# Kernel tuning notes

Measured on AMD Instinct MI355X. Metric: run time of the kernel, lower is better.

The kernel has to match this reference:

```python
import jax, jax.numpy as jnp
import numpy as np

HID = 128
NLAYERS = 8
LAT = 32
DIM_IN = 63 + 15 + LAT  # pe(xyz,L=10)=3+60, pe(shift,L=2)=3+12, latent=32 -> 110


def _pe(x, L):
    # NeRF positional encoding, include_input=True, freq-major [sin3,cos3] per freq
    freqs = (2.0 ** jnp.arange(L)).astype(x.dtype)
    xf = x[..., None, :] * freqs[:, None]                      # [..., L, 3]
    sc = jnp.concatenate([jnp.sin(xf), jnp.cos(xf)], axis=-1)  # [..., L, 6]
    return jnp.concatenate([x, sc.reshape(*x.shape[:-1], 6 * L)], axis=-1)


def setup_inputs() -> dict:
    key = jax.random.key(0)
    ks = jax.random.split(key, 24)
    B, P, V = 2, 32768, 5023
    d = {}
    d["pts"] = jax.random.normal(ks[0], (B, P, 3), jnp.float32)
    d["deformed_mesh_pts"] = jax.random.normal(ks[1], (B, V, 3), jnp.float32)
    d["cano_verts"] = jax.random.normal(ks[2], (1, V, 3), jnp.float32)
    d["motion_latent"] = jax.random.normal(ks[3], (B, P, LAT), jnp.float32)
    for i in range(NLAYERS):
        fin = DIM_IN if i == 0 else (DIM_IN + HID if i == NLAYERS // 2 else HID)
        d[f"w{i}"] = jax.random.normal(ks[4 + i], (HID, fin), jnp.float32) / np.sqrt(fin).astype(np.float32)
        d[f"b{i}"] = jnp.zeros((HID,), jnp.float32)
    d["w_out"] = jax.random.normal(ks[20], (3, HID), jnp.float32) * 0.01
    d["b_out"] = jnp.zeros((3,), jnp.float32)
    return d


def reference(pts, deformed_mesh_pts, cano_verts, motion_latent,
              w0, b0, w1, b1, w2, b2, w3, b3, w4, b4, w5, b5, w6, b6, w7, b7,
              w_out, b_out):
    # mesh-guided shift per vertex
    mesh_shift = cano_verts - deformed_mesh_pts                 # [B,V,3]
    # point-to-point NN search (squared euclidean cdist + argmin)
    d2 = ((pts ** 2).sum(-1)[:, :, None]
          + (deformed_mesh_pts ** 2).sum(-1)[:, None, :]
          - 2.0 * jnp.einsum('bpc,bvc->bpv', pts, deformed_mesh_pts))  # [B,P,V]
    d2 = jnp.maximum(d2, 0.0)
    idx = jnp.argmin(d2, axis=-1)                               # [B,P]
    dist = jnp.min(d2, axis=-1)                                 # [B,P]
    weight = jnp.exp(-dist)[..., None]                          # 1/exp(dist)
    gidx = jnp.broadcast_to(idx[:, :, None], idx.shape + (3,))
    gshift = jnp.take_along_axis(mesh_shift, gidx, axis=1) * weight  # [B,P,3]
    # deformation MLP with skip connection at layer 4
    initial = jnp.concatenate([_pe(pts, 10), _pe(gshift, 2), motion_latent], axis=-1)
    ws = [w0, w1, w2, w3, w4, w5, w6, w7]
    bs = [b0, b1, b2, b3, b4, b5, b6, b7]
    x = initial
    last_feat = x
    for i in range(NLAYERS):
        inp = jnp.concatenate([initial, x], axis=-1) if i == NLAYERS // 2 else x
        x = inp @ ws[i].T + bs[i]
        last_feat = x  # pre-activation feature (out_feat_ls[-1])
        x = jax.nn.relu(x)
    mlp_shift = x @ w_out.T + b_out                             # [B,P,3]
    pts_shifts = gshift + mlp_shift
    return pts + pts_shifts, last_feat
```

## Files before the change

### kernel.cpp

```cpp
#include <hip/hip_runtime.h>
#include <math.h>

typedef unsigned short ushort_t;
typedef unsigned int   uint_t;
typedef __attribute__((ext_vector_type(8)))  short bf16x8;
typedef __attribute__((ext_vector_type(16))) float f32x16;

#define NPTS   65536
#define NV     5023
#define NVP    5120
#define NTILE  160
#define LATD   32
#define KF     110
#define FSTR   112
#define MARGIN 1.5e-2f

union U4 { uint_t u[4]; bf16x8 v; };

__device__ __forceinline__ ushort_t f2bf(float f) {
  union { float f; unsigned u; } x; x.f = f;
  unsigned r = x.u + 0x7fffu + ((x.u >> 16) & 1u);
  return (ushort_t)(r >> 16);
}
__device__ __forceinline__ float bf2f(ushort_t u) {
  union { unsigned u; float f; } x; x.u = ((unsigned)u) << 16;
  return x.f;
}
__device__ __forceinline__ uint_t packsplit(float v) {
  const ushort_t h = f2bf(v);
  const ushort_t l = f2bf(v - bf2f(h));
  return (uint_t)h | ((uint_t)l << 16);
}

__device__ __forceinline__ void dbl_step(float& s, float& c) {
  const float t = s * c;
  const float cn = fmaf(-2.f * s, s, 1.f);
  s = t + t;
  c = cn;
}

__global__ __launch_bounds__(256) void k_prep(
    const float* __restrict__ dm,
    const float* __restrict__ w0, const float* __restrict__ w1,
    const float* __restrict__ w2, const float* __restrict__ w3,
    const float* __restrict__ w4, const float* __restrict__ w5,
    const float* __restrict__ w6, const float* __restrict__ w7,
    ushort_t* __restrict__ wsWh, ushort_t* __restrict__ wsWl,
    ushort_t* __restrict__ aFF, ushort_t* __restrict__ aFH,
    float4* __restrict__ vq)
{
  const int e = blockIdx.x * 256 + threadIdx.x;
  {
    const int p = e >> 14, local = e & 16383;
    const int j   = local & 7;
    const int lh  = (local >> 3) & 1;
    const int l31 = (local >> 4) & 31;
    const int tn  = (local >> 9) & 3;
    const int ks  = (local >> 11) & 7;
    const int n = tn*32 + l31;
    const int k = ks*16 + lh*8 + j;
    float v;
    if (p == 0)      v = (k < KF) ? w0[n*110 + k] : 0.f;
    else if (p == 1) v = w1[n*128 + k];
    else if (p == 2) v = w2[n*128 + k];
    else if (p == 3) v = w3[n*128 + k];
    else if (p == 4) v = (k < KF) ? w4[n*238 + k] : 0.f;
    else if (p == 5) v = w4[n*238 + KF + k];
    else if (p == 6) v = w5[n*128 + k];
    else if (p == 7) v = w6[n*128 + k];
    else             v = w7[n*128 + k];
    const ushort_t h = f2bf(v);
    wsWh[e] = h;
    wsWl[e] = f2bf(v - bf2f(h));
  }
  if (e < 2*NVP) {
    const int b = (e >= NVP) ? 1 : 0;
    const int v = e - b*NVP;
    const float* __restrict__ dmb = dm + b*NV*3;
    float x = 0.f, y = 0.f, z = 0.f, wv = 3.0e38f;
    if (v < NV) {
      x = dmb[v*3+0]; y = dmb[v*3+1]; z = dmb[v*3+2];
      wv = fmaf(x,x, fmaf(y,y, z*z));
    }
    const ushort_t hx = f2bf(x),  hy = f2bf(y),  hz = f2bf(z),  hw = f2bf(wv);
    const ushort_t lx = f2bf(x - bf2f(hx)), ly = f2bf(y - bf2f(hy));
    const ushort_t lz = f2bf(z - bf2f(hz)), lw = f2bf(wv - bf2f(hw));
    U4 F, H;
    F.u[0] = (uint_t)hx | ((uint_t)hy << 16);
    F.u[1] = (uint_t)hz | ((uint_t)hw << 16);
    F.u[2] = (uint_t)lx | ((uint_t)ly << 16);
    F.u[3] = (uint_t)lz | ((uint_t)lw << 16);
    H.u[0] = F.u[0]; H.u[1] = F.u[1]; H.u[2] = 0; H.u[3] = 0;
    *(bf16x8*)(aFF + (size_t)e*8) = F.v;
    *(bf16x8*)(aFH + (size_t)e*8) = H.v;
    vq[e] = make_float4(x, y, z, wv);
  }
}

__device__ __forceinline__ float min16(const f32x16& d) {
  const float t0 = fminf(fminf(d[0],d[1]),   fminf(d[2],d[3]));
  const float t1 = fminf(fminf(d[4],d[5]),   fminf(d[6],d[7]));
  const float t2 = fminf(fminf(d[8],d[9]),   fminf(d[10],d[11]));
  const float t3 = fminf(fminf(d[12],d[13]), fminf(d[14],d[15]));
  return fminf(fminf(t0,t1), fminf(t2,t3));
}

__global__ __launch_bounds__(256, 2) void k_nnfeat(
    const float* __restrict__ pts, const float* __restrict__ dm,
    const float* __restrict__ cano, const float* __restrict__ lat,
    const ushort_t* __restrict__ aFF, const ushort_t* __restrict__ aFH,
    const float4* __restrict__ vq,
    uint_t* __restrict__ feat, float* __restrict__ base3)
{
  __shared__ float sD[128];
  __shared__ int   sI[128];

  const int tid = threadIdx.x;
  const int lane = tid & 63, w = tid >> 6;
  const int l31 = lane & 31, lh = lane >> 5;
  const int g0 = blockIdx.x * 128;
  const int b  = blockIdx.x >> 8;
  const int pt = g0 + w*32 + l31;

  const float px = pts[pt*3+0], py = pts[pt*3+1], pz = pts[pt*3+2];
  const float p2 = fmaf(px,px, fmaf(py,py, pz*pz));

  const float tpx = -2.f*px, tpy = -2.f*py, tpz = -2.f*pz;
  const ushort_t hpx = f2bf(tpx), hpy = f2bf(tpy), hpz = f2bf(tpz);
  const ushort_t lpx = f2bf(tpx - bf2f(hpx));
  const ushort_t lpy = f2bf(tpy - bf2f(hpy));
  const ushort_t lpz = f2bf(tpz - bf2f(hpz));
  U4 Bh, Bl;
  Bh.u[0] = (uint_t)hpx | ((uint_t)hpy << 16);
  Bh.u[1] = (uint_t)hpz | (0x3F80u << 16);
  Bh.u[2] = Bh.u[0]; Bh.u[3] = Bh.u[1];
  Bl.u[0] = (uint_t)lpx | ((uint_t)lpy << 16);
  Bl.u[1] = (uint_t)lpz;
  Bl.u[2] = 0; Bl.u[3] = 0;
  const bf16x8 bfrag = lh ? Bl.v : Bh.v;

  const ushort_t* __restrict__ aBase = (lh ? aFH : aFF) + (size_t)b * NVP * 8;
  const float4*   __restrict__ vqb   = vq + (size_t)b * NVP;

  const f32x16 zacc = (f32x16)(0.f);

  float gmin = 3.0e38f;
  bf16x8 ap0, ap1, ap2, ap3, an0, an1, an2, an3;
  ap0 = *(const bf16x8*)(aBase + (size_t)(0*32 + l31)*8);
  ap1 = *(const bf16x8*)(aBase + (size_t)(1*32 + l31)*8);
  ap2 = *(const bf16x8*)(aBase + (size_t)(2*32 + l31)*8);
  ap3 = *(const bf16x8*)(aBase + (size_t)(3*32 + l31)*8);
  #pragma unroll 2
  for (int tb = 0; tb < 40; ++tb) {
    const int t0 = tb*4;
    if (tb + 1 < 40) {
      an0 = *(const bf16x8*)(aBase + (size_t)((t0+4)*32 + l31)*8);
      an1 = *(const bf16x8*)(aBase + (size_t)((t0+5)*32 + l31)*8);
      an2 = *(const bf16x8*)(aBase + (size_t)((t0+6)*32 + l31)*8);
      an3 = *(const bf16x8*)(aBase + (size_t)((t0+7)*32 + l31)*8);
    }
    const f32x16 d0 = __builtin_amdgcn_mfma_f32_32x32x16_bf16(ap0, bfrag, zacc, 0,0,0);
    const f32x16 d1 = __builtin_amdgcn_mfma_f32_32x32x16_bf16(ap1, bfrag, zacc, 0,0,0);
    const f32x16 d2 = __builtin_amdgcn_mfma_f32_32x32x16_bf16(ap2, bfrag, zacc, 0,0,0);
    const f32x16 d3 = __builtin_amdgcn_mfma_f32_32x32x16_bf16(ap3, bfrag, zacc, 0,0,0);
    const float m0 = min16(d0), m1 = min16(d1), m2 = min16(d2), m3 = min16(d3);
    gmin = fminf(gmin, fminf(fminf(m0,m1), fminf(m2,m3)));
    ap0 = an0; ap1 = an1; ap2 = an2; ap3 = an3;
  }
  gmin = fminf(gmin, __shfl_xor(gmin, 32, 64));
  const float thr = gmin + MARGIN;

  float bs = 3.4e38f; int bi = 0;
  ap0 = *(const bf16x8*)(aBase + (size_t)(0*32 + l31)*8);
  ap1 = *(const bf16x8*)(aBase + (size_t)(1*32 + l31)*8);
  ap2 = *(const bf16x8*)(aBase + (size_t)(2*32 + l31)*8);
  ap3 = *(const bf16x8*)(aBase + (size_t)(3*32 + l31)*8);
  #pragma unroll 1
  for (int tb = 0; tb < 40; ++tb) {
    const int t0 = tb*4;
    if (tb + 1 < 40) {
      an0 = *(const bf16x8*)(aBase + (size_t)((t0+4)*32 + l31)*8);
      an1 = *(const bf16x8*)(aBase + (size_t)((t0+5)*32 + l31)*8);
      an2 = *(const bf16x8*)(aBase + (size_t)((t0+6)*32 + l31)*8);
      an3 = *(const bf16x8*)(aBase + (size_t)((t0+7)*32 + l31)*8);
    }
    f32x16 dd[4];
    dd[0] = __builtin_amdgcn_mfma_f32_32x32x16_bf16(ap0, bfrag, zacc, 0,0,0);
    dd[1] = __builtin_amdgcn_mfma_f32_32x32x16_bf16(ap1, bfrag, zacc, 0,0,0);
    dd[2] = __builtin_amdgcn_mfma_f32_32x32x16_bf16(ap2, bfrag, zacc, 0,0,0);
    dd[3] = __builtin_amdgcn_mfma_f32_32x32x16_bf16(ap3, bfrag, zacc, 0,0,0);
    #pragma unroll
    for (int i = 0; i < 4; ++i) {
      const f32x16 d = dd[i];
      float q4[4];
      q4[0] = fminf(fminf(d[0],d[1]),   fminf(d[2],d[3]));
      q4[1] = fminf(fminf(d[4],d[5]),   fminf(d[6],d[7]));
      q4[2] = fminf(fminf(d[8],d[9]),   fminf(d[10],d[11]));
      q4[3] = fminf(fminf(d[12],d[13]), fminf(d[14],d[15]));
      const float tm = fminf(fminf(q4[0],q4[1]), fminf(q4[2],q4[3]));
      if (tm <= thr) {
        const int t = t0 + i;
        #pragma unroll
        for (int q = 0; q < 4; ++q) {
          if (q4[q] <= thr) {
            #pragma unroll
            for (int rr = 0; rr < 4; ++rr) {
              const int r = q*4 + rr;
              if (d[r] <= thr) {
                const int row = (r & 3) + 8*(r >> 2) + 4*lh;
                const int v = t*32 + row;
                const float4 qv = vqb[v];
                const float dot = fmaf(px, qv.x, fmaf(py, qv.y, pz*qv.z));
                float d2 = fmaf(-2.f, dot, p2 + qv.w);
                d2 = fmaxf(d2, 0.f);
                if (d2 < bs || (d2 == bs && v < bi)) { bs = d2; bi = v; }
              }
            }
          }
        }
      }
    }
    ap0 = an0; ap1 = an1; ap2 = an2; ap3 = an3;
  }
  {
    const float ob = __shfl_xor(bs, 32, 64);
    const int   oi = __shfl_xor(bi, 32, 64);
    if (ob < bs || (ob == bs && oi < bi)) { bs = ob; bi = oi; }
  }
  if (lh == 0) { sD[w*32 + l31] = bs; sI[w*32 + l31] = bi; }
  __syncthreads();

  const int p = tid & 127, slice = tid >> 7;
  const int g = g0 + p;
  const float wd = sD[p];
  const int   wi = sI[p];
  const float* __restrict__ dmb = dm + b * NV * 3;

  const float qx = pts[g*3+0], qy = pts[g*3+1], qz = pts[g*3+2];
  const float wgt = expf(-wd);
  const float sx = (cano[wi*3+0] - dmb[wi*3+0]) * wgt;
  const float sy = (cano[wi*3+1] - dmb[wi*3+1]) * wgt;
  const float sz = (cano[wi*3+2] - dmb[wi*3+2]) * wgt;

  uint_t* __restrict__ fr = feat + (size_t)g * FSTR;

  if (slice == 0) {
    base3[g*3+0] = qx + sx; base3[g*3+1] = qy + sy; base3[g*3+2] = qz + sz;
    fr[0] = packsplit(qx); fr[1] = packsplit(qy); fr[2] = packsplit(qz);
    float s0,c0,s1,c1,s2,c2;
    sincosf(qx,&s0,&c0); sincosf(qy,&s1,&c1); sincosf(qz,&s2,&c2);
    #pragma unroll
    for (int f = 0; f < 3; ++f) {
      const int k = 3 + 6*f;
      fr[k+0]=packsplit(s0); fr[k+1]=packsplit(s1); fr[k+2]=packsplit(s2);
      fr[k+3]=packsplit(c0); fr[k+4]=packsplit(c1); fr[k+5]=packsplit(c2);
      if (f < 2) { dbl_step(s0,c0); dbl_step(s1,c1); dbl_step(s2,c2); }
    }
    sincosf(qx*8.f,&s0,&c0); sincosf(qy*8.f,&s1,&c1); sincosf(qz*8.f,&s2,&c2);
    #pragma unroll
    for (int f = 3; f < 7; ++f) {
      const int k = 3 + 6*f;
      fr[k+0]=packsplit(s0); fr[k+1]=packsplit(s1); fr[k+2]=packsplit(s2);
      fr[k+3]=packsplit(c0); fr[k+4]=packsplit(c1); fr[k+5]=packsplit(c2);
      if (f < 6) { dbl_step(s0,c0); dbl_step(s1,c1); dbl_step(s2,c2); }
    }
  } else {
    float s0,c0,s1,c1,s2,c2;
    sincosf(qx*128.f,&s0,&c0); sincosf(qy*128.f,&s1,&c1); sincosf(qz*128.f,&s2,&c2);
    #pragma unroll
    for (int f = 7; f < 10; ++f) {
      const int k = 3 + 6*f;
      fr[k+0]=packsplit(s0); fr[k+1]=packsplit(s1); fr[k+2]=packsplit(s2);
      fr[k+3]=packsplit(c0); fr[k+4]=packsplit(c1); fr[k+5]=packsplit(c2);
      if (f < 9) { dbl_step(s0,c0); dbl_step(s1,c1); dbl_step(s2,c2); }
    }
    fr[63]=packsplit(sx); fr[64]=packsplit(sy); fr[65]=packsplit(sz);
    sincosf(sx,&s0,&c0); sincosf(sy,&s1,&c1); sincosf(sz,&s2,&c2);
    #pragma unroll
    for (int f = 0; f < 2; ++f) {
      const int k = 66 + 6*f;
      fr[k+0]=packsplit(s0); fr[k+1]=packsplit(s1); fr[k+2]=packsplit(s2);
      fr[k+3]=packsplit(c0); fr[k+4]=packsplit(c1); fr[k+5]=packsplit(c2);
      if (f < 1) { dbl_step(s0,c0); dbl_step(s1,c1); dbl_step(s2,c2); }
    }
    #pragma unroll
    for (int j = 0; j < 32; ++j) fr[78+j] = packsplit(lat[g*LATD + j]);
    fr[110] = 0; fr[111] = 0;
  }
}


__device__ __forceinline__ void zero4(f32x16 (&a)[4]) {
  #pragma unroll
  for (int i = 0; i < 4; ++i) a[i] = (f32x16)(0.f);
}

__device__ __forceinline__ void load_feat_frags(
    const uint_t* __restrict__ fr, bf16x8 (&Xh)[8], bf16x8 (&Xl)[8], int lh)
{
  #pragma unroll
  for (int ks = 0; ks < 7; ++ks) {
    const int k0 = ks*16 + lh*8;
    const uint4 ua = *(const uint4*)(fr + k0);
    const uint4 ub = *(const uint4*)(fr + k0 + 4);
    U4 H, L;
    H.u[0] = (ua.x & 0xffffu) | (ua.y << 16);
    H.u[1] = (ua.z & 0xffffu) | (ua.w << 16);
    H.u[2] = (ub.x & 0xffffu) | (ub.y << 16);
    H.u[3] = (ub.z & 0xffffu) | (ub.w << 16);
    L.u[0] = (ua.x >> 16) | (ua.y & 0xffff0000u);
    L.u[1] = (ua.z >> 16) | (ua.w & 0xffff0000u);
    L.u[2] = (ub.x >> 16) | (ub.y & 0xffff0000u);
    L.u[3] = (ub.z >> 16) | (ub.w & 0xffff0000u);
    Xh[ks] = H.v; Xl[ks] = L.v;
  }
}

__device__ __forceinline__ void load_slab(bf16x8 (&wh)[4], bf16x8 (&wl)[4],
    const ushort_t* __restrict__ Wh, const ushort_t* __restrict__ Wl,
    int ks, int l31, int lh)
{
  const int lo = l31*16 + lh*8;
  #pragma unroll
  for (int tn = 0; tn < 4; ++tn) {
    const int off = (ks*4 + tn)*512 + lo;
    wh[tn] = *(const bf16x8*)(Wh + off);
    wl[tn] = *(const bf16x8*)(Wl + off);
  }
}

__device__ __forceinline__ void mfma_slab(f32x16 (&acc)[4],
    const bf16x8 (&wh)[4], const bf16x8 (&wl)[4],
    const bf16x8& xh, const bf16x8& xl)
{
  #pragma unroll
  for (int tn = 0; tn < 4; ++tn) {
    acc[tn] = __builtin_amdgcn_mfma_f32_32x32x16_bf16(wh[tn], xh, acc[tn], 0,0,0);
    acc[tn] = __builtin_amdgcn_mfma_f32_32x32x16_bf16(wl[tn], xh, acc[tn], 0,0,0);
    acc[tn] = __builtin_amdgcn_mfma_f32_32x32x16_bf16(wh[tn], xl, acc[tn], 0,0,0);
  }
}

template<int NKS, bool TAIL>
__device__ __forceinline__ void run_panel(f32x16 (&acc)[4],
    const ushort_t* __restrict__ Wh, const ushort_t* __restrict__ Wl,
    const ushort_t* __restrict__ WhN, const ushort_t* __restrict__ WlN,
    bf16x8 (&wbh)[2][4], bf16x8 (&wbl)[2][4],
    const bf16x8 (&Xh)[8], const bf16x8 (&Xl)[8], int l31, int lh)
{
  #pragma unroll
  for (int ks = 0; ks < NKS; ++ks) {
    const int b = ks & 1;
    mfma_slab(acc, wbh[b], wbl[b], Xh[ks], Xl[ks]);
    if (ks + 2 < NKS) {
      load_slab(wbh[b], wbl[b], Wh, Wl, ks + 2, l31, lh);
    } else if (TAIL) {
      load_slab(wbh[b], wbl[b], WhN, WlN, ks & 1, l31, lh);
    }
  }
}

__device__ __forceinline__ void bias_relu(f32x16 (&acc)[4],
    const float* __restrict__ bias, int lh)
{
  #pragma unroll
  for (int tn = 0; tn < 4; ++tn)
    #pragma unroll
    for (int b = 0; b < 4; ++b) {
      const float4 b4 = *(const float4*)(bias + tn*32 + 8*b + 4*lh);
      acc[tn][4*b+0] = fmaxf(acc[tn][4*b+0] + b4.x, 0.f);
      acc[tn][4*b+1] = fmaxf(acc[tn][4*b+1] + b4.y, 0.f);
      acc[tn][4*b+2] = fmaxf(acc[tn][4*b+2] + b4.z, 0.f);
      acc[tn][4*b+3] = fmaxf(acc[tn][4*b+3] + b4.w, 0.f);
    }
}

__device__ __forceinline__ void build_frags(const f32x16 (&acc)[4],
    bf16x8 (&Xh)[8], bf16x8 (&Xl)[8], int lh)
{
  #pragma unroll
  for (int ks = 0; ks < 8; ++ks) {
    const int tn = ks >> 1;
    const int rb = 8*(ks & 1);
    const float f0 = acc[tn][rb+0], f1 = acc[tn][rb+1];
    const float f2 = acc[tn][rb+2], f3 = acc[tn][rb+3];
    const float f4 = acc[tn][rb+4], f5 = acc[tn][rb+5];
    const float f6 = acc[tn][rb+6], f7 = acc[tn][rb+7];
    const ushort_t h0=f2bf(f0), h1=f2bf(f1), h2=f2bf(f2), h3=f2bf(f3);
    const ushort_t h4=f2bf(f4), h5=f2bf(f5), h6=f2bf(f6), h7=f2bf(f7);
    const uint_t hA0 = (uint_t)h0 | ((uint_t)h1 << 16);
    const uint_t hA1 = (uint_t)h2 | ((uint_t)h3 << 16);
    const uint_t hB0 = (uint_t)h4 | ((uint_t)h5 << 16);
    const uint_t hB1 = (uint_t)h6 | ((uint_t)h7 << 16);
    const uint_t lA0 = (uint_t)f2bf(f0 - bf2f(h0)) | ((uint_t)f2bf(f1 - bf2f(h1)) << 16);
    const uint_t lA1 = (uint_t)f2bf(f2 - bf2f(h2)) | ((uint_t)f2bf(f3 - bf2f(h3)) << 16);
    const uint_t lB0 = (uint_t)f2bf(f4 - bf2f(h4)) | ((uint_t)f2bf(f5 - bf2f(h5)) << 16);
    const uint_t lB1 = (uint_t)f2bf(f6 - bf2f(h6)) | ((uint_t)f2bf(f7 - bf2f(h7)) << 16);
    const uint_t sh0 = lh ? hA0 : hB0, sh1 = lh ? hA1 : hB1;
    const uint_t sl0 = lh ? lA0 : lB0, sl1 = lh ? lA1 : lB1;
    const uint_t rh0 = __shfl_xor(sh0, 32, 64), rh1 = __shfl_xor(sh1, 32, 64);
    const uint_t rl0 = __shfl_xor(sl0, 32, 64), rl1 = __shfl_xor(sl1, 32, 64);
    U4 H, L;
    H.u[0] = lh ? rh0 : hA0;  H.u[1] = lh ? rh1 : hA1;
    H.u[2] = lh ? hB0 : rh0;  H.u[3] = lh ? hB1 : rh1;
    L.u[0] = lh ? rl0 : lA0;  L.u[1] = lh ? rl1 : lA1;
    L.u[2] = lh ? lB0 : rl0;  L.u[3] = lh ? lB1 : rl1;
    Xh[ks] = H.v; Xl[ks] = L.v;
  }
}

__global__ __launch_bounds__(256, 2) void k_mlp(
    const uint_t* __restrict__ feat, const float* __restrict__ base3,
    const ushort_t* __restrict__ wsWh, const ushort_t* __restrict__ wsWl,
    const float* __restrict__ b0, const float* __restrict__ b1,
    const float* __restrict__ b2, const float* __restrict__ b3,
    const float* __restrict__ b4, const float* __restrict__ b5,
    const float* __restrict__ b6, const float* __restrict__ b7,
    const float* __restrict__ w_out, const float* __restrict__ b_out,
    float* __restrict__ out)
{
  __shared__ __align__(16) float sF[4][32*132];
  __shared__ __align__(16) float sB[8*128 + 384 + 4];

  const int tid  = threadIdx.x;
  const int lane = tid & 63, wid = tid >> 6;
  const int l31 = lane & 31, lh = lane >> 5;
  const int p0 = blockIdx.x * 128 + wid * 32;

  {
    const float* bsp[8] = {b0,b1,b2,b3,b4,b5,b6,b7};
    if (tid < 128) {
      #pragma unroll
      for (int l = 0; l < 8; ++l) sB[l*128 + tid] = bsp[l][tid];
    }
    for (int i = tid; i < 384; i += 256) sB[1024 + i] = w_out[i];
    if (tid < 3) sB[1408 + tid] = b_out[tid];
  }

  const uint_t* __restrict__ fr = feat + (size_t)(p0 + l31) * FSTR;

  bf16x8 Xh[8], Xl[8];
  bf16x8 wbh[2][4], wbl[2][4];
  f32x16 acc[4];

  load_slab(wbh[0], wbl[0], wsWh, wsWl, 0, l31, lh);
  load_slab(wbh[1], wbl[1], wsWh, wsWl, 1, l31, lh);
  load_feat_frags(fr, Xh, Xl, lh);
  __syncthreads();

  zero4(acc);
  run_panel<7,true>(acc, wsWh + 0*16384, wsWl + 0*16384,
                         wsWh + 1*16384, wsWl + 1*16384, wbh, wbl, Xh, Xl, l31, lh);
  bias_relu(acc, sB + 0*128, lh);
  build_frags(acc, Xh, Xl, lh);

  zero4(acc);
  run_panel<8,true>(acc, wsWh + 1*16384, wsWl + 1*16384,
                         wsWh + 2*16384, wsWl + 2*16384, wbh, wbl, Xh, Xl, l31, lh);
  bias_relu(acc, sB + 1*128, lh);
  build_frags(acc, Xh, Xl, lh);

  zero4(acc);
  run_panel<8,true>(acc, wsWh + 2*16384, wsWl + 2*16384,
                         wsWh + 3*16384, wsWl + 3*16384, wbh, wbl, Xh, Xl, l31, lh);
  bias_relu(acc, sB + 2*128, lh);
  build_frags(acc, Xh, Xl, lh);

  zero4(acc);
  run_panel<8,true>(acc, wsWh + 3*16384, wsWl + 3*16384,
                         wsWh + 5*16384, wsWl + 5*16384, wbh, wbl, Xh, Xl, l31, lh);
  bias_relu(acc, sB + 3*128, lh);
  build_frags(acc, Xh, Xl, lh);

  zero4(acc);
  run_panel<8,true>(acc, wsWh + 5*16384, wsWl + 5*16384,
                         wsWh + 4*16384, wsWl + 4*16384, wbh, wbl, Xh, Xl, l31, lh);
  load_feat_frags(fr, Xh, Xl, lh);
  run_panel<7,true>(acc, wsWh + 4*16384, wsWl + 4*16384,
                         wsWh + 6*16384, wsWl + 6*16384, wbh, wbl, Xh, Xl, l31, lh);
  bias_relu(acc, sB + 4*128, lh);
  build_frags(acc, Xh, Xl, lh);

  zero4(acc);
  run_panel<8,true>(acc, wsWh + 6*16384, wsWl + 6*16384,
                         wsWh + 7*16384, wsWl + 7*16384, wbh, wbl, Xh, Xl, l31, lh);
  bias_relu(acc, sB + 5*128, lh);
  build_frags(acc, Xh, Xl, lh);

  zero4(acc);
  run_panel<8,true>(acc, wsWh + 7*16384, wsWl + 7*16384,
                         wsWh + 8*16384, wsWl + 8*16384, wbh, wbl, Xh, Xl, l31, lh);
  bias_relu(acc, sB + 6*128, lh);
  build_frags(acc, Xh, Xl, lh);

  zero4(acc);
  run_panel<8,false>(acc, wsWh + 8*16384, wsWl + 8*16384,
                          (const ushort_t*)0, (const ushort_t*)0, wbh, wbl, Xh, Xl, l31, lh);

  float* __restrict__ sFw = &sF[wid][0];
  #pragma unroll
  for (int tn = 0; tn < 4; ++tn)
    #pragma unroll
    for (int b = 0; b < 4; ++b) {
      const int n0 = tn*32 + 8*b + 4*lh;
      const float4 bv = *(const float4*)(sB + 7*128 + n0);
      const float v0 = acc[tn][4*b+0] + bv.x;
      const float v1 = acc[tn][4*b+1] + bv.y;
      const float v2 = acc[tn][4*b+2] + bv.z;
      const float v3 = acc[tn][4*b+3] + bv.w;
      *(float4*)(sFw + l31*132 + n0) = make_float4(v0, v1, v2, v3);
      acc[tn][4*b+0] = fmaxf(v0, 0.f);
      acc[tn][4*b+1] = fmaxf(v1, 0.f);
      acc[tn][4*b+2] = fmaxf(v2, 0.f);
      acc[tn][4*b+3] = fmaxf(v3, 0.f);
    }

  asm volatile("s_waitcnt lgkmcnt(0)" ::: "memory");
  __builtin_amdgcn_sched_barrier(0);

  float* __restrict__ out1 = out + (size_t)NPTS * 3;
  #pragma unroll
  for (int i = 0; i < 16; ++i) {
    const int idx = i*64 + lane;
    const int p = idx >> 5, q = idx & 31;
    const float4 v = *(const float4*)(sFw + p*132 + q*4);
    *(float4*)(out1 + (size_t)(p0 + p)*128 + q*4) = v;
  }

  float dotc[3];
  #pragma unroll
  for (int c = 0; c < 3; ++c) {
    float a = 0.f;
    #pragma unroll
    for (int tn = 0; tn < 4; ++tn)
      #pragma unroll
      for (int b = 0; b < 4; ++b) {
        const int n0 = tn*32 + 8*b + 4*lh;
        const float4 w4 = *(const float4*)(sB + 1024 + c*128 + n0);
        a = fmaf(acc[tn][4*b+0], w4.x, a);
        a = fmaf(acc[tn][4*b+1], w4.y, a);
        a = fmaf(acc[tn][4*b+2], w4.z, a);
        a = fmaf(acc[tn][4*b+3], w4.w, a);
      }
    a += __shfl_xor(a, 32, 64);
    dotc[c] = a;
  }
  if (lh == 0) {
    const int g = p0 + l31;
    #pragma unroll
    for (int c = 0; c < 3; ++c)
      out[g*3 + c] = base3[g*3 + c] + dotc[c] + sB[1408 + c];
  }
}

extern "C" void kernel_launch(void* const* d_in, const int* in_sizes, int n_in,
                              void* d_out, int out_size, void* d_ws, size_t ws_size,
                              hipStream_t stream)
{
  const float* pts  = (const float*)d_in[0];
  const float* dm   = (const float*)d_in[1];
  const float* cano = (const float*)d_in[2];
  const float* lat  = (const float*)d_in[3];
  const float* w[8]; const float* b[8];
  for (int i = 0; i < 8; ++i) {
    w[i] = (const float*)d_in[4 + 2*i];
    b[i] = (const float*)d_in[5 + 2*i];
  }
  const float* w_out = (const float*)d_in[20];
  const float* b_out = (const float*)d_in[21];
  float* out = (float*)d_out;

  uint_t*   feat  = (uint_t*)d_ws;
  float*    base3 = (float*)((char*)d_ws + (size_t)NPTS*FSTR*4);
  ushort_t* wsWh  = (ushort_t*)((char*)base3 + (size_t)NPTS*3*4);
  ushort_t* wsWl  = wsWh + 147456;
  ushort_t* aFF   = wsWl + 147456;
  ushort_t* aFH   = aFF + 2*NVP*8;
  float4*   vq    = (float4*)(aFH + 2*NVP*8);

  k_prep<<<576, 256, 0, stream>>>(dm,
      w[0],w[1],w[2],w[3],w[4],w[5],w[6],w[7], wsWh, wsWl, aFF, aFH, vq);
  k_nnfeat<<<512, 256, 0, stream>>>(pts, dm, cano, lat, aFF, aFH, vq, feat, base3);
  k_mlp<<<NPTS/128, 256, 0, stream>>>(feat, base3, wsWh, wsWl,
      b[0],b[1],b[2],b[3],b[4],b[5],b[6],b[7], w_out, b_out, out);
}
```

Before: 246.0 us.

## Split NN vertex scan across two waves per point group and double grid

Each block now handles 64 points instead of 128. The two wave pairs each scan half of the padded vertex tiles for the same 32 points, then combine per-half minima through shared memory to form the threshold and the final argmin. The feature-encoding epilogue is redistributed over four 64-thread slices, and launch bounds rise to 4 blocks/SM with twice the grid. This aims to raise parallelism and occupancy for the per-point serial scan at the cost of an extra block barrier, shared-memory reductions, and tighter register budgets.

```diff
diff --git a/kernel.cpp b/kernel.cpp
--- a/kernel.cpp
+++ b/kernel.cpp
@@ -10,6 +10,7 @@
 #define NV     5023
 #define NVP    5120
 #define NTILE  160
+#define HTILE  80
 #define LATD   32
 #define KF     110
 #define FSTR   112
@@ -105,22 +106,25 @@
   return fminf(fminf(t0,t1), fminf(t2,t3));
 }
 
-__global__ __launch_bounds__(256, 2) void k_nnfeat(
+__global__ __launch_bounds__(256, 4) void k_nnfeat(
     const float* __restrict__ pts, const float* __restrict__ dm,
     const float* __restrict__ cano, const float* __restrict__ lat,
     const ushort_t* __restrict__ aFF, const ushort_t* __restrict__ aFH,
     const float4* __restrict__ vq,
     uint_t* __restrict__ feat, float* __restrict__ base3)
 {
-  __shared__ float sD[128];
-  __shared__ int   sI[128];
+  __shared__ float sMin[2][64];
+  __shared__ float sDh[2][64];
+  __shared__ int   sIh[2][64];
 
   const int tid = threadIdx.x;
   const int lane = tid & 63, w = tid >> 6;
   const int l31 = lane & 31, lh = lane >> 5;
-  const int g0 = blockIdx.x * 128;
-  const int b  = blockIdx.x >> 8;
-  const int pt = g0 + w*32 + l31;
+  const int half = w & 1, pg = w >> 1;
+  const int g0 = blockIdx.x * 64;
+  const int b  = blockIdx.x >> 9;
+  const int pt = g0 + pg*32 + l31;
+  const int pidx = pg*32 + l31;
 
   const float px = pts[pt*3+0], py = pts[pt*3+1], pz = pts[pt*3+2];
   const float p2 = fmaf(px,px, fmaf(py,py, pz*pz));
@@ -139,8 +143,10 @@
   Bl.u[2] = 0; Bl.u[3] = 0;
   const bf16x8 bfrag = lh ? Bl.v : Bh.v;
 
-  const ushort_t* __restrict__ aBase = (lh ? aFH : aFF) + (size_t)b * NVP * 8;
+  const ushort_t* __restrict__ aBase = (lh ? aFH : aFF)
+      + (size_t)b * NVP * 8 + (size_t)half * HTILE * 32 * 8;
   const float4*   __restrict__ vqb   = vq + (size_t)b * NVP;
+  const int vho = half * HTILE * 32;
 
   const f32x16 zacc = (f32x16)(0.f);
 
@@ -151,9 +157,9 @@
   ap2 = *(const bf16x8*)(aBase + (size_t)(2*32 + l31)*8);
   ap3 = *(const bf16x8*)(aBase + (size_t)(3*32 + l31)*8);
   #pragma unroll 2
-  for (int tb = 0; tb < 40; ++tb) {
+  for (int tb = 0; tb < HTILE/4; ++tb) {
     const int t0 = tb*4;
-    if (tb + 1 < 40) {
+    if (tb + 1 < HTILE/4) {
       an0 = *(const bf16x8*)(aBase + (size_t)((t0+4)*32 + l31)*8);
       an1 = *(const bf16x8*)(aBase + (size_t)((t0+5)*32 + l31)*8);
       an2 = *(const bf16x8*)(aBase + (size_t)((t0+6)*32 + l31)*8);
@@ -168,7 +174,9 @@
     ap0 = an0; ap1 = an1; ap2 = an2; ap3 = an3;
   }
   gmin = fminf(gmin, __shfl_xor(gmin, 32, 64));
-  const float thr = gmin + MARGIN;
+  if (lh == 0) sMin[half][pidx] = gmin;
+  __syncthreads();
+  const float thr = fminf(sMin[0][pidx], sMin[1][pidx]) + MARGIN;
 
   float bs = 3.4e38f; int bi = 0;
   ap0 = *(const bf16x8*)(aBase + (size_t)(0*32 + l31)*8);
@@ -176,9 +184,9 @@
   ap2 = *(const bf16x8*)(aBase + (size_t)(2*32 + l31)*8);
   ap3 = *(const bf16x8*)(aBase + (size_t)(3*32 + l31)*8);
   #pragma unroll 1
-  for (int tb = 0; tb < 40; ++tb) {
+  for (int tb = 0; tb < HTILE/4; ++tb) {
     const int t0 = tb*4;
-    if (tb + 1 < 40) {
+    if (tb + 1 < HTILE/4) {
       an0 = *(const bf16x8*)(aBase + (size_t)((t0+4)*32 + l31)*8);
       an1 = *(const bf16x8*)(aBase + (size_t)((t0+5)*32 + l31)*8);
       an2 = *(const bf16x8*)(aBase + (size_t)((t0+6)*32 + l31)*8);
@@ -208,7 +216,7 @@
               const int r = q*4 + rr;
               if (d[r] <= thr) {
                 const int row = (r & 3) + 8*(r >> 2) + 4*lh;
-                const int v = t*32 + row;
+                const int v = vho + t*32 + row;
                 const float4 qv = vqb[v];
                 const float dot = fmaf(px, qv.x, fmaf(py, qv.y, pz*qv.z));
                 float d2 = fmaf(-2.f, dot, p2 + qv.w);
@@ -227,13 +235,16 @@
     const int   oi = __shfl_xor(bi, 32, 64);
     if (ob < bs || (ob == bs && oi < bi)) { bs = ob; bi = oi; }
   }
-  if (lh == 0) { sD[w*32 + l31] = bs; sI[w*32 + l31] = bi; }
+  if (lh == 0) { sDh[half][pidx] = bs; sIh[half][pidx] = bi; }
   __syncthreads();
 
-  const int p = tid & 127, slice = tid >> 7;
+  const int p = tid & 63, slice = tid >> 6;
   const int g = g0 + p;
-  const float wd = sD[p];
-  const int   wi = sI[p];
+  float wd = sDh[0][p]; int wi = sIh[0][p];
+  {
+    const float od = sDh[1][p]; const int oi = sIh[1][p];
+    if (od < wd || (od == wd && oi < wi)) { wd = od; wi = oi; }
+  }
   const float* __restrict__ dmb = dm + b * NV * 3;
 
   const float qx = pts[g*3+0], qy = pts[g*3+1], qz = pts[g*3+2];
@@ -256,6 +267,9 @@
       fr[k+3]=packsplit(c0); fr[k+4]=packsplit(c1); fr[k+5]=packsplit(c2);
       if (f < 2) { dbl_step(s0,c0); dbl_step(s1,c1); dbl_step(s2,c2); }
     }
+    fr[110] = 0; fr[111] = 0;
+  } else if (slice == 1) {
+    float s0,c0,s1,c1,s2,c2;
     sincosf(qx*8.f,&s0,&c0); sincosf(qy*8.f,&s1,&c1); sincosf(qz*8.f,&s2,&c2);
     #pragma unroll
     for (int f = 3; f < 7; ++f) {
@@ -264,7 +278,7 @@
       fr[k+3]=packsplit(c0); fr[k+4]=packsplit(c1); fr[k+5]=packsplit(c2);
       if (f < 6) { dbl_step(s0,c0); dbl_step(s1,c1); dbl_step(s2,c2); }
     }
-  } else {
+  } else if (slice == 2) {
     float s0,c0,s1,c1,s2,c2;
     sincosf(qx*128.f,&s0,&c0); sincosf(qy*128.f,&s1,&c1); sincosf(qz*128.f,&s2,&c2);
     #pragma unroll
@@ -274,7 +288,11 @@
       fr[k+3]=packsplit(c0); fr[k+4]=packsplit(c1); fr[k+5]=packsplit(c2);
       if (f < 9) { dbl_step(s0,c0); dbl_step(s1,c1); dbl_step(s2,c2); }
     }
+    #pragma unroll
+    for (int j = 0; j < 16; ++j) fr[78+j] = packsplit(lat[g*LATD + j]);
+  } else {
     fr[63]=packsplit(sx); fr[64]=packsplit(sy); fr[65]=packsplit(sz);
+    float s0,c0,s1,c1,s2,c2;
     sincosf(sx,&s0,&c0); sincosf(sy,&s1,&c1); sincosf(sz,&s2,&c2);
     #pragma unroll
     for (int f = 0; f < 2; ++f) {
@@ -284,8 +302,7 @@
       if (f < 1) { dbl_step(s0,c0); dbl_step(s1,c1); dbl_step(s2,c2); }
     }
     #pragma unroll
-    for (int j = 0; j < 32; ++j) fr[78+j] = packsplit(lat[g*LATD + j]);
-    fr[110] = 0; fr[111] = 0;
+    for (int j = 16; j < 32; ++j) fr[78+j] = packsplit(lat[g*LATD + j]);
   }
 }
 
@@ -580,7 +597,7 @@
 
   k_prep<<<576, 256, 0, stream>>>(dm,
       w[0],w[1],w[2],w[3],w[4],w[5],w[6],w[7], wsWh, wsWl, aFF, aFH, vq);
-  k_nnfeat<<<512, 256, 0, stream>>>(pts, dm, cano, lat, aFF, aFH, vq, feat, base3);
+  k_nnfeat<<<1024, 256, 0, stream>>>(pts, dm, cano, lat, aFF, aFH, vq, feat, base3);
   k_mlp<<<NPTS/128, 256, 0, stream>>>(feat, base3, wsWh, wsWl,
       b[0],b[1],b[2],b[3],b[4],b[5],b[6],b[7], w_out, b_out, out);
 }
```

After: 232.1 us. 5.6% less time.
